# Kernel optimization log

Hardware: AMD Instinct MI355X
Metric: run time of the kernel (lower is better)

The kernel has to match this reference:

```python
import jax, jax.numpy as jnp
import numpy as np

B, L, D_MODEL = 2, 1024, 1024
D_STATE, D_CONV, EXPAND = 16, 4, 2
D_INNER = D_MODEL * EXPAND
LN_EPS = 1e-5


def setup_inputs() -> dict:
    key = jax.random.key(0)
    ks = jax.random.split(key, 6)
    g = lambda k, shape, scale: (jax.random.normal(k, shape, jnp.float32) * scale)
    x = jax.random.normal(ks[0], (B, L, D_MODEL), jnp.float32)
    in_proj_w = g(ks[1], (2 * D_INNER, D_MODEL), D_MODEL ** -0.5)
    conv_w = g(ks[2], (D_INNER, D_CONV), D_CONV ** -0.5)   # depthwise kernel
    conv_b = jnp.zeros((D_INNER,), jnp.float32)
    x_proj_w = g(ks[3], (2 * D_STATE + 1, D_INNER), D_INNER ** -0.5)
    A_log = jnp.tile(jnp.log(jnp.arange(1, D_STATE + 1, dtype=jnp.float32)), (D_INNER, 1))
    D_param = jnp.ones((D_INNER,), jnp.float32)
    dt_w = g(ks[4], (D_INNER, 1), 1.0)
    dt_b = jnp.full((D_INNER,), -4.0, jnp.float32)
    out_w = g(ks[5], (D_MODEL, D_INNER), D_INNER ** -0.5)
    ln_g = jnp.ones((D_INNER,), jnp.float32)
    ln_b = jnp.zeros((D_INNER,), jnp.float32)
    return dict(x=x, in_proj_w=in_proj_w, conv_w=conv_w, conv_b=conv_b,
                x_proj_w=x_proj_w, A_log=A_log, D_param=D_param,
                dt_w=dt_w, dt_b=dt_b, out_w=out_w, ln_g=ln_g, ln_b=ln_b)


def _forward(x, in_proj_w, conv_w, conv_b, x_proj_w, A_log, D_param,
             dt_w, dt_b, out_w, ln_g, ln_b):
    Lq = x.shape[1]
    xz = jnp.einsum('bld,ed->ble', x, in_proj_w)            # (B,L,2*Di)
    xb, z = xz[..., :D_INNER], xz[..., D_INNER:]
    # causal depthwise conv1d (pad left d_conv-1, valid conv == torch pad+truncate)
    xpad = jnp.pad(xb, ((0, 0), (D_CONV - 1, 0), (0, 0)))
    xc = conv_b
    for k in range(D_CONV):
        xc = xc + xpad[:, k:k + Lq, :] * conv_w[:, k]
    xb = jax.nn.silu(xc)
    proj = jnp.einsum('bld,ed->ble', xb, x_proj_w)          # (B,L,2N+1)
    dt_in = proj[..., :1]
    Bp = proj[..., 1:1 + D_STATE]                            # (B,L,N)
    Cp = proj[..., 1 + D_STATE:]                             # (B,L,N)
    dt = jax.nn.softplus(dt_in * dt_w[:, 0] + dt_b)          # (B,L,Di)
    A = -jnp.exp(A_log)                                      # (Di,N)
    dA = jnp.exp(dt[..., None] * A)                          # (B,L,Di,N)
    x_scaled = (xb * dt)[..., None] * Bp[..., None, :]       # (B,L,Di,N)
    # linear recurrence h[t] = dA[t]*h[t-1] + x_scaled[t] via associative scan
    def comb(a, b):
        return (a[0] * b[0], b[0] * a[1] + b[1])
    _, h = jax.lax.associative_scan(comb, (dA, x_scaled), axis=1)
    y = jnp.einsum('bldn,bln->bld', h, Cp) + xb * D_param    # (B,L,Di)
    mu = jnp.mean(y, axis=-1, keepdims=True)
    var = jnp.var(y, axis=-1, keepdims=True)
    y = (y - mu) / jnp.sqrt(var + LN_EPS) * ln_g + ln_b
    y = y * jax.nn.silu(z)
    return jnp.einsum('bld,ed->ble', y, out_w)               # (B,L,d_model)


def reference(x, in_proj_w, conv_w, conv_b, x_proj_w, A_log, D_param,
              dt_w, dt_b, out_w, ln_g, ln_b):
    return _forward(x, in_proj_w, conv_w, conv_b, x_proj_w, A_log, D_param,
                    dt_w, dt_b, out_w, ln_g, ln_b)
```

## Files before the change

### kernel.cpp

```cpp
#include <hip/hip_runtime.h>

typedef unsigned short u16;
typedef unsigned int u32;
typedef __bf16 bf16x8 __attribute__((ext_vector_type(8)));
typedef float f32x4 __attribute__((ext_vector_type(4)));
typedef unsigned short ushort8 __attribute__((ext_vector_type(8)));

__device__ __forceinline__ float bf2f(u16 b) {
    return __uint_as_float(((u32)b) << 16);
}
__device__ __forceinline__ u16 f2bf(float f) {
    u32 u = __float_as_uint(f);
    return (u16)((u + 0x7fffu + ((u >> 16) & 1u)) >> 16);
}

#define P_CONVW 0
#define P_CONVB 8192
#define P_ALOG  10240
#define P_DPAR  43008
#define P_DTW   45056
#define P_DTB   47104
#define P_LNG   49152
#define P_LNB   51200
#define P_TOTAL 53248

#define CCH 32
#define CT  32
#define CHUNKTOT 2097152
#define PSTRIDE 128

#define CV_X   524288
#define CV_W1  1572864
#define CV_TOT 2097152

struct ParamPtrs { const void* p[8]; };

__global__ __launch_bounds__(256) void canon_all(ParamPtrs pp, float* __restrict__ cpar,
                                                 const void* __restrict__ sx,
                                                 const void* __restrict__ sw1,
                                                 const void* __restrict__ swo,
                                                 u16* __restrict__ cx,
                                                 const void* __restrict__ sxp,
                                                 u16* __restrict__ wpad,
                                                 float* __restrict__ proj,
                                                 float* __restrict__ dout,
                                                 const u16* __restrict__ dp) {
    const bool isbf = (dp[0] != 0);
    const int blk = blockIdx.x;
    const int tid = threadIdx.x;
    if (blk < 8192) {
        const int i = blk * 256 + tid;
        const void* src;
        int off;
        if (i < CV_X)       { src = sx;  off = i; }
        else if (i < CV_W1) { src = sw1; off = i - CV_X; }
        else                { src = swo; off = i - CV_W1; }
        if (isbf) {
            ((uint2*)cx)[i] = ((const uint2*)src)[off];
        } else {
            const float4 v = ((const float4*)src)[off];
            uint2 o;
            o.x = (u32)f2bf(v.x) | ((u32)f2bf(v.y) << 16);
            o.y = (u32)f2bf(v.z) | ((u32)f2bf(v.w) << 16);
            ((uint2*)cx)[i] = o;
        }
    } else if (blk < 8400) {
        const int i = (blk - 8192) * 256 + tid;
        int seg, off;
        if (i < P_CONVB)      { seg = 0; off = i; }
        else if (i < P_ALOG)  { seg = 1; off = i - P_CONVB; }
        else if (i < P_DPAR)  { seg = 2; off = i - P_ALOG; }
        else if (i < P_DTW)   { seg = 3; off = i - P_DPAR; }
        else if (i < P_DTB)   { seg = 4; off = i - P_DTW; }
        else if (i < P_LNG)   { seg = 5; off = i - P_DTB; }
        else if (i < P_LNB)   { seg = 6; off = i - P_LNG; }
        else                  { seg = 7; off = i - P_LNB; }
        cpar[i] = isbf ? bf2f(((const u16*)pp.p[seg])[off]) : ((const float*)pp.p[seg])[off];
    } else if (blk < 8656) {
        const int i = (blk - 8400) * 256 + tid;
        const int idx = i * 4;
        const int row = idx >> 11;
        u16 o[4];
#pragma unroll
        for (int q = 0; q < 4; ++q) {
            float v = 0.f;
            if (row < 33)
                v = isbf ? bf2f(((const u16*)sxp)[idx + q]) : ((const float*)sxp)[idx + q];
            o[q] = f2bf(v);
        }
        *(uint2*)&wpad[idx] = *(uint2*)o;
    } else if (blk < 8912) {
        const int i = (blk - 8656) * 256 + tid;
        ((float4*)proj)[i] = make_float4(0.f, 0.f, 0.f, 0.f);
    } else {
        const int i = (blk - 8912) * 256 + tid;
        ((float4*)dout)[i] = make_float4(0.f, 0.f, 0.f, 0.f);
    }
}

template <int MODE>
__global__ __launch_bounds__(256) void gemm_bt(const u16* __restrict__ A,
                                               const u16* __restrict__ Bw,
                                               void* __restrict__ C,
                                               int M, int N, int Kseg,
                                               int lda, int ldb) {
    const int bm = blockIdx.x;
    const int bn = blockIdx.y;
    const int kbase = blockIdx.z * Kseg;
    const int tid = threadIdx.x;
    const int lane = tid & 63;
    const int wave = tid >> 6;
    const int wm = wave >> 1, wn = wave & 1;
    const int l16 = lane & 15, quad = lane >> 4;

    __shared__ __align__(16) u16 sA[128 * 32];
    __shared__ __align__(16) u16 sB[128 * 32];

    f32x4 acc[4][4] = {};

    const int rsub = lane >> 2;
    const int csub = (lane & 3) * 8;

    for (int k0 = 0; k0 < Kseg; k0 += 32) {
        const int kc = kbase + k0 + csub;
        __syncthreads();
#pragma unroll
        for (int q = 0; q < 2; ++q) {
            const int g = wave + 4 * q;
            const int row = g * 16 + rsub;
            __builtin_amdgcn_global_load_lds(
                (const u32*)&A[(size_t)(bm * 128 + row) * lda + kc],
                (u32*)&sA[g * 512], 16, 0, 0);
            __builtin_amdgcn_global_load_lds(
                (const u32*)&Bw[(size_t)(bn * 128 + row) * ldb + kc],
                (u32*)&sB[g * 512], 16, 0, 0);
        }
        __syncthreads();

        bf16x8 af[4], bg[4];
#pragma unroll
        for (int t = 0; t < 4; ++t) {
            af[t] = *(const bf16x8*)&sA[(wm * 64 + t * 16 + l16) * 32 + quad * 8];
            bg[t] = *(const bf16x8*)&sB[(wn * 64 + t * 16 + l16) * 32 + quad * 8];
        }
#pragma unroll
        for (int mt = 0; mt < 4; ++mt)
#pragma unroll
            for (int nt = 0; nt < 4; ++nt)
                acc[mt][nt] = __builtin_amdgcn_mfma_f32_16x16x32_bf16(
                    af[mt], bg[nt], acc[mt][nt], 0, 0, 0);
    }

    float* Cf = (float*)C + (MODE == 1 ? (size_t)blockIdx.z * M * N : (size_t)0);
#pragma unroll
    for (int mt = 0; mt < 4; ++mt) {
#pragma unroll
        for (int r = 0; r < 4; ++r) {
            const int row = bm * 128 + wm * 64 + mt * 16 + quad * 4 + r;
#pragma unroll
            for (int nt = 0; nt < 4; ++nt) {
                const int col = bn * 128 + wn * 64 + nt * 16 + l16;
                if (MODE == 0)
                    ((u16*)C)[(size_t)row * N + col] = f2bf(acc[mt][nt][r]);
                else if (MODE == 1)
                    Cf[(size_t)row * N + col] = acc[mt][nt][r];
                else
                    unsafeAtomicAdd(&Cf[(size_t)row * N + col], acc[mt][nt][r]);
            }
        }
    }
}

__global__ __launch_bounds__(256) void conv_silu(const u16* __restrict__ xz,
                                                 const float* __restrict__ par,
                                                 u16* __restrict__ xb16) {
    const int idx = blockIdx.x * 256 + threadIdx.x;
    const int d8 = idx & 255;
    const int bl = idx >> 8;
    const int l = bl & 1023;
    const int d0 = d8 * 8;

    float acc[8];
    {
        const float4 b0 = *(const float4*)&par[P_CONVB + d0];
        const float4 b1 = *(const float4*)&par[P_CONVB + d0 + 4];
        acc[0] = b0.x; acc[1] = b0.y; acc[2] = b0.z; acc[3] = b0.w;
        acc[4] = b1.x; acc[5] = b1.y; acc[6] = b1.z; acc[7] = b1.w;
    }
    float warr[8][4];
#pragma unroll
    for (int q = 0; q < 8; ++q) {
        const float4 w = *(const float4*)&par[P_CONVW + (d0 + q) * 4];
        warr[q][0] = w.x; warr[q][1] = w.y; warr[q][2] = w.z; warr[q][3] = w.w;
    }
#pragma unroll
    for (int k = 0; k < 4; ++k) {
        const int ls = l + k - 3;
        if (ls >= 0) {
            const ushort8 xv = *(const ushort8*)&xz[(size_t)(bl + k - 3) * 4096 + d0];
#pragma unroll
            for (int q = 0; q < 8; ++q)
                acc[q] = fmaf(bf2f(xv[q]), warr[q][k], acc[q]);
        }
    }
    u16 o[8];
#pragma unroll
    for (int q = 0; q < 8; ++q) {
        const float s = acc[q] / (1.f + __expf(-acc[q]));
        o[q] = f2bf(s);
    }
    *(uint4*)&xb16[(size_t)bl * 2048 + d0] = *(uint4*)o;
}

__global__ __launch_bounds__(256) void scan_p1(const u16* __restrict__ xb16,
                                               const float* __restrict__ proj,
                                               const float* __restrict__ par,
                                               float* __restrict__ PS) {
    const int d = blockIdx.x * 256 + threadIdx.x;
    const int c = blockIdx.y;
    const int b = blockIdx.z;
    __shared__ float sp[CT][33];
    const size_t row0 = (size_t)b * 1024 + c * CT;
    for (int f = threadIdx.x; f < CT * 33; f += 256) {
        const int i = f / 33, j = f - i * 33;
        sp[i][j] = proj[(row0 + i) * PSTRIDE + j];
    }
    float Aneg[16];
#pragma unroll
    for (int n = 0; n < 16; ++n) Aneg[n] = -__expf(par[P_ALOG + d * 16 + n]);
    const float dtw = par[P_DTW + d], dtb = par[P_DTB + d];
    __syncthreads();

    float h[16] = {}, P[16];
#pragma unroll
    for (int n = 0; n < 16; ++n) P[n] = 1.f;

    float xv = bf2f(xb16[row0 * 2048 + d]);
    for (int i = 0; i < CT; ++i) {
        const float xv_next = (i + 1 < CT) ? bf2f(xb16[(row0 + i + 1) * 2048 + d]) : 0.f;
        const float dtin = sp[i][0];
        const float darg = fmaf(dtin, dtw, dtb);
        const float dt = (darg > 20.f) ? darg : __logf(1.f + __expf(darg));
        const float xdt = xv * dt;
#pragma unroll
        for (int n = 0; n < 16; ++n) {
            const float dA = __expf(dt * Aneg[n]);
            P[n] *= dA;
            h[n] = fmaf(dA, h[n], xdt * sp[i][1 + n]);
        }
        xv = xv_next;
    }
    const size_t base = (((size_t)b * CCH + c) * 16) * 2048 + d;
#pragma unroll
    for (int n = 0; n < 16; ++n) {
        PS[base + (size_t)n * 2048] = P[n];
        PS[CHUNKTOT + base + (size_t)n * 2048] = h[n];
    }
}

__global__ __launch_bounds__(256) void scan_comb(const float* __restrict__ PS,
                                                 float* __restrict__ H) {
    const int t = blockIdx.x * 256 + threadIdx.x;
    const int d = t & 2047;
    const int n = (t >> 11) & 15;
    const int b = t >> 15;
    float h = 0.f;
#pragma unroll
    for (int c = 0; c < CCH; ++c) {
        const size_t idx = (((size_t)b * CCH + c) * 16 + n) * 2048 + d;
        H[idx] = h;
        h = fmaf(PS[idx], h, PS[CHUNKTOT + idx]);
    }
}

__global__ __launch_bounds__(256) void scan_p2(const u16* __restrict__ xb16,
                                               const float* __restrict__ proj,
                                               const float* __restrict__ par,
                                               const float* __restrict__ H,
                                               u16* __restrict__ y) {
    const int d = blockIdx.x * 256 + threadIdx.x;
    const int c = blockIdx.y;
    const int b = blockIdx.z;
    __shared__ float sp[CT][33];
    const size_t row0 = (size_t)b * 1024 + c * CT;
    for (int f = threadIdx.x; f < CT * 33; f += 256) {
        const int i = f / 33, j = f - i * 33;
        sp[i][j] = proj[(row0 + i) * PSTRIDE + j];
    }
    float Aneg[16], h[16];
    const size_t hbase = (((size_t)b * CCH + c) * 16) * 2048 + d;
#pragma unroll
    for (int n = 0; n < 16; ++n) {
        Aneg[n] = -__expf(par[P_ALOG + d * 16 + n]);
        h[n] = H[hbase + (size_t)n * 2048];
    }
    const float dtw = par[P_DTW + d], dtb = par[P_DTB + d];
    const float Dp = par[P_DPAR + d];
    __syncthreads();

    float xv = bf2f(xb16[row0 * 2048 + d]);
    for (int i = 0; i < CT; ++i) {
        const float xv_next = (i + 1 < CT) ? bf2f(xb16[(row0 + i + 1) * 2048 + d]) : 0.f;
        const float dtin = sp[i][0];
        const float darg = fmaf(dtin, dtw, dtb);
        const float dt = (darg > 20.f) ? darg : __logf(1.f + __expf(darg));
        const float xdt = xv * dt;
        float acc = 0.f;
#pragma unroll
        for (int n = 0; n < 16; ++n) {
            const float dA = __expf(dt * Aneg[n]);
            h[n] = fmaf(dA, h[n], xdt * sp[i][1 + n]);
            acc = fmaf(h[n], sp[i][17 + n], acc);
        }
        y[(row0 + i) * 2048 + d] = f2bf(fmaf(xv, Dp, acc));
        xv = xv_next;
    }
}

__global__ __launch_bounds__(256) void ln_silu(const u16* __restrict__ y,
                                               const u16* __restrict__ xz,
                                               const float* __restrict__ par,
                                               u16* __restrict__ yn) {
    const int row = blockIdx.x;
    const int tid = threadIdx.x;
    const int lane = tid & 63, wave = tid >> 6;
    const int d0 = tid * 8;
    const ushort8 vy = *(const ushort8*)&y[(size_t)row * 2048 + d0];
    float v[8];
    float s = 0.f, s2 = 0.f;
#pragma unroll
    for (int i = 0; i < 8; ++i) {
        v[i] = bf2f(vy[i]);
        s += v[i];
        s2 = fmaf(v[i], v[i], s2);
    }
    s += __shfl_xor(s, 1); s2 += __shfl_xor(s2, 1);
    s += __shfl_xor(s, 2); s2 += __shfl_xor(s2, 2);
    s += __shfl_xor(s, 4); s2 += __shfl_xor(s2, 4);
    s += __shfl_xor(s, 8); s2 += __shfl_xor(s2, 8);
    s += __shfl_xor(s, 16); s2 += __shfl_xor(s2, 16);
    s += __shfl_xor(s, 32); s2 += __shfl_xor(s2, 32);
    __shared__ float rs[4], rs2[4];
    if (lane == 0) { rs[wave] = s; rs2[wave] = s2; }
    __syncthreads();
    const float ts = rs[0] + rs[1] + rs[2] + rs[3];
    const float ts2 = rs2[0] + rs2[1] + rs2[2] + rs2[3];
    const float mu = ts * (1.f / 2048.f);
    const float var = ts2 * (1.f / 2048.f) - mu * mu;
    const float rstd = rsqrtf(var + 1e-5f);

    const ushort8 vz = *(const ushort8*)&xz[(size_t)row * 4096 + 2048 + d0];
    float g[8], bb[8];
    {
        const float4 g0 = *(const float4*)&par[P_LNG + d0];
        const float4 g1 = *(const float4*)&par[P_LNG + d0 + 4];
        g[0] = g0.x; g[1] = g0.y; g[2] = g0.z; g[3] = g0.w;
        g[4] = g1.x; g[5] = g1.y; g[6] = g1.z; g[7] = g1.w;
        const float4 b0 = *(const float4*)&par[P_LNB + d0];
        const float4 b1 = *(const float4*)&par[P_LNB + d0 + 4];
        bb[0] = b0.x; bb[1] = b0.y; bb[2] = b0.z; bb[3] = b0.w;
        bb[4] = b1.x; bb[5] = b1.y; bb[6] = b1.z; bb[7] = b1.w;
    }
    u16 o[8];
#pragma unroll
    for (int i = 0; i < 8; ++i) {
        float t = (v[i] - mu) * rstd * g[i] + bb[i];
        const float z = bf2f(vz[i]);
        t *= z / (1.f + __expf(-z));
        o[i] = f2bf(t);
    }
    *(uint4*)&yn[(size_t)row * 2048 + d0] = *(uint4*)o;
}

extern "C" void kernel_launch(void* const* d_in, const int* in_sizes, int n_in,
                              void* d_out, int out_size, void* d_ws, size_t ws_size,
                              hipStream_t stream) {
    const void* x         = d_in[0];
    const void* in_proj_w = d_in[1];
    const void* conv_w    = d_in[2];
    const void* conv_b    = d_in[3];
    const void* x_proj_w  = d_in[4];
    const void* A_log     = d_in[5];
    const void* D_param   = d_in[6];
    const void* dt_w      = d_in[7];
    const void* dt_b      = d_in[8];
    const void* out_w     = d_in[9];
    const void* ln_g      = d_in[10];
    const void* ln_b      = d_in[11];
    const u16* dp = (const u16*)D_param;

    float* cpar = (float*)d_ws;
    u16* cx     = (u16*)(cpar + P_TOTAL);
    u16* cw1    = cx + 2097152;
    u16* cwo    = cw1 + 4194304;
    u16* xz     = cwo + 2097152;
    u16* xb16   = xz + 8388608;
    u16* y      = xb16 + 4194304;
    u16* wpad   = y + 4194304;
    float* proj = (float*)(wpad + 262144);
    float* PS   = proj + 262144;
    float* H    = PS + 2 * CHUNKTOT;
    u16* yn     = xb16;

    ParamPtrs pp;
    pp.p[0] = conv_w; pp.p[1] = conv_b; pp.p[2] = A_log; pp.p[3] = D_param;
    pp.p[4] = dt_w;   pp.p[5] = dt_b;   pp.p[6] = ln_g;  pp.p[7] = ln_b;
    canon_all<<<10960, 256, 0, stream>>>(pp, cpar, x, in_proj_w, out_w, cx,
                                         x_proj_w, wpad, proj, (float*)d_out, dp);

    gemm_bt<0><<<dim3(16, 32, 1), 256, 0, stream>>>(cx, cw1, xz, 2048, 4096, 1024, 1024, 1024);
    conv_silu<<<2048, 256, 0, stream>>>(xz, cpar, xb16);
    gemm_bt<2><<<dim3(16, 1, 8), 256, 0, stream>>>(xb16, wpad, proj, 2048, 128, 256, 2048, 2048);
    scan_p1<<<dim3(8, CCH, 2), 256, 0, stream>>>(xb16, proj, cpar, PS);
    scan_comb<<<256, 256, 0, stream>>>(PS, H);
    scan_p2<<<dim3(8, CCH, 2), 256, 0, stream>>>(xb16, proj, cpar, H, y);
    ln_silu<<<2048, 256, 0, stream>>>(y, xz, cpar, yn);
    gemm_bt<2><<<dim3(16, 8, 2), 256, 0, stream>>>(yn, cwo, (float*)d_out, 2048, 1024, 1024, 2048, 2048);
}
```

Before: 255.4 us.

## Add triple-buffered direct-to-LDS GEMM and replace atomic split-K with partial reductions

Adds a new 512-thread GEMM kernel that loads tiles straight into swizzled LDS through global_load_lds, keeps three LDS stages in flight, and interleaves fragment reads with MFMA under raised wave priority. It uses 128x256 tiles and is used for the input and output projections. Split-K results for x_proj and out_proj are now written as separate partial buffers and summed by a new reduce kernel, replacing float atomics and the zero-init in canon_all. The cost is more LDS per block (144KB), extra workspace for the partials, and two extra kernel launches.

```diff
diff --git a/kernel.cpp b/kernel.cpp
--- a/kernel.cpp
+++ b/kernel.cpp
@@ -42,8 +42,6 @@
                                                  u16* __restrict__ cx,
                                                  const void* __restrict__ sxp,
                                                  u16* __restrict__ wpad,
-                                                 float* __restrict__ proj,
-                                                 float* __restrict__ dout,
                                                  const u16* __restrict__ dp) {
     const bool isbf = (dp[0] != 0);
     const int blk = blockIdx.x;
@@ -76,7 +74,7 @@
         else if (i < P_LNB)   { seg = 6; off = i - P_LNG; }
         else                  { seg = 7; off = i - P_LNB; }
         cpar[i] = isbf ? bf2f(((const u16*)pp.p[seg])[off]) : ((const float*)pp.p[seg])[off];
-    } else if (blk < 8656) {
+    } else {
         const int i = (blk - 8400) * 256 + tid;
         const int idx = i * 4;
         const int row = idx >> 11;
@@ -89,12 +87,132 @@
             o[q] = f2bf(v);
         }
         *(uint2*)&wpad[idx] = *(uint2*)o;
-    } else if (blk < 8912) {
-        const int i = (blk - 8656) * 256 + tid;
-        ((float4*)proj)[i] = make_float4(0.f, 0.f, 0.f, 0.f);
-    } else {
-        const int i = (blk - 8912) * 256 + tid;
-        ((float4*)dout)[i] = make_float4(0.f, 0.f, 0.f, 0.f);
+    }
+}
+
+__device__ __forceinline__ bf16x8 lds_frag(const char* smem, u32 base, int row, int kk,
+                                           int quad, u32 xorv) {
+    const u32 addr = (base + (u32)(row * 128 + kk * 64 + quad * 16)) ^ xorv;
+    return *(const bf16x8*)(smem + addr);
+}
+
+template <int MODE>
+__global__ __launch_bounds__(512, 2) void gemm8(const u16* __restrict__ A,
+                                                const u16* __restrict__ Bw,
+                                                void* __restrict__ C,
+                                                int M, int N, int Kseg,
+                                                int lda, int ldb) {
+    extern __shared__ char smem[];
+    const int bm = blockIdx.x, bn = blockIdx.y;
+    const int kbase = blockIdx.z * Kseg;
+    const int tid = threadIdx.x;
+    const int lane = tid & 63, wave = tid >> 6;
+    const int wm = wave >> 2, wn = wave & 3;
+    const int l16 = lane & 15, quad = lane >> 4;
+    const int NT = Kseg >> 6;
+    const u32 xorv = (u32)((l16 & 7) << 4);
+
+    const int rIss = wave * 8 + (lane >> 3);
+    const int logC = (lane & 7) ^ ((lane >> 3) & 7);
+    size_t aSrc[2], bSrc[4];
+#pragma unroll
+    for (int j = 0; j < 2; ++j)
+        aSrc[j] = (size_t)(bm * 128 + j * 64 + rIss) * lda + logC * 8 + kbase;
+#pragma unroll
+    for (int j = 0; j < 4; ++j)
+        bSrc[j] = (size_t)(bn * 256 + j * 64 + rIss) * ldb + logC * 8 + kbase;
+    const u32 ldsW = (u32)(wave * 1024);
+
+#define SG_A(slot, j, kel) __builtin_amdgcn_global_load_lds( \
+        (const u32*)(A + aSrc[j] + (kel)), (u32*)(smem + (slot) + (j) * 8192 + ldsW), 16, 0, 0)
+#define SG_B(slot, j, kel) __builtin_amdgcn_global_load_lds( \
+        (const u32*)(Bw + bSrc[j] + (kel)), (u32*)(smem + (slot) + (j) * 8192 + ldsW), 16, 0, 0)
+
+    const u32 sA0 = 0, sA1 = 16384, sA2 = 32768;
+    const u32 sB0 = 49152, sB1 = 81920, sB2 = 114688;
+
+    SG_A(sA0, 0, 0); SG_A(sA0, 1, 0);
+    SG_B(sB0, 0, 0); SG_B(sB0, 1, 0); SG_B(sB0, 2, 0); SG_B(sB0, 3, 0);
+    SG_A(sA1, 0, 64); SG_A(sA1, 1, 64);
+    SG_B(sB1, 0, 64); SG_B(sB1, 1, 64); SG_B(sB1, 2, 64); SG_B(sB1, 3, 64);
+    asm volatile("s_waitcnt vmcnt(6)" ::: "memory");
+    __builtin_amdgcn_s_barrier();
+    __builtin_amdgcn_sched_barrier(0);
+
+    u32 curA = sA0, nxtA = sA1, stgA = sA2;
+    u32 curB = sB0, nxtB = sB1, stgB = sB2;
+    int kStage = 128;
+
+    f32x4 acc[4][4] = {};
+    bf16x8 a[4][2], b[4][2];
+
+    for (int t = 0; t < NT; ++t) {
+        const bool doStage = (t + 2) < NT;
+#pragma unroll
+        for (int mt = 0; mt < 4; ++mt)
+#pragma unroll
+            for (int kk = 0; kk < 2; ++kk)
+                a[mt][kk] = lds_frag(smem, curA, wm * 64 + mt * 16 + l16, kk, quad, xorv);
+#pragma unroll
+        for (int nt = 0; nt < 2; ++nt)
+#pragma unroll
+            for (int kk = 0; kk < 2; ++kk)
+                b[nt][kk] = lds_frag(smem, curB, wn * 64 + nt * 16 + l16, kk, quad, xorv);
+        if (doStage) { SG_A(stgA, 0, kStage); SG_A(stgA, 1, kStage); SG_B(stgB, 0, kStage); }
+        __builtin_amdgcn_s_setprio(1);
+#pragma unroll
+        for (int mt = 0; mt < 4; ++mt)
+#pragma unroll
+            for (int nt = 0; nt < 2; ++nt)
+#pragma unroll
+                for (int kk = 0; kk < 2; ++kk)
+                    acc[mt][nt] = __builtin_amdgcn_mfma_f32_16x16x32_bf16(
+                        a[mt][kk], b[nt][kk], acc[mt][nt], 0, 0, 0);
+        __builtin_amdgcn_s_setprio(0);
+#pragma unroll
+        for (int nt = 2; nt < 4; ++nt)
+#pragma unroll
+            for (int kk = 0; kk < 2; ++kk)
+                b[nt][kk] = lds_frag(smem, curB, wn * 64 + nt * 16 + l16, kk, quad, xorv);
+        if (doStage) { SG_B(stgB, 1, kStage); SG_B(stgB, 2, kStage); SG_B(stgB, 3, kStage); }
+        __builtin_amdgcn_s_setprio(1);
+#pragma unroll
+        for (int mt = 0; mt < 4; ++mt)
+#pragma unroll
+            for (int nt = 2; nt < 4; ++nt)
+#pragma unroll
+                for (int kk = 0; kk < 2; ++kk)
+                    acc[mt][nt] = __builtin_amdgcn_mfma_f32_16x16x32_bf16(
+                        a[mt][kk], b[nt][kk], acc[mt][nt], 0, 0, 0);
+        __builtin_amdgcn_s_setprio(0);
+        if (t < NT - 1) {
+            if (doStage) asm volatile("s_waitcnt vmcnt(6)" ::: "memory");
+            else         asm volatile("s_waitcnt vmcnt(0)" ::: "memory");
+            __builtin_amdgcn_s_barrier();
+            __builtin_amdgcn_sched_barrier(0);
+            u32 tA = curA; curA = nxtA; nxtA = stgA; stgA = tA;
+            u32 tB = curB; curB = nxtB; nxtB = stgB; stgB = tB;
+            kStage += 64;
+        }
+    }
+#undef SG_A
+#undef SG_B
+
+    float* Cf = (float*)C + (MODE == 1 ? (size_t)blockIdx.z * M * N : (size_t)0);
+#pragma unroll
+    for (int mt = 0; mt < 4; ++mt) {
+#pragma unroll
+        for (int r = 0; r < 4; ++r) {
+            const int row = bm * 128 + wm * 64 + mt * 16 + quad * 4 + r;
+#pragma unroll
+            for (int nt = 0; nt < 4; ++nt) {
+                const int col = bn * 256 + wn * 64 + nt * 16 + l16;
+                if (MODE == 0)
+                    ((u16*)C)[(size_t)row * N + col] = f2bf(acc[mt][nt][r]);
+                else
+                    Cf[(size_t)row * N + col] = acc[mt][nt][r];
+            }
+        }
     }
 }
 
@@ -162,13 +280,24 @@
                 const int col = bn * 128 + wn * 64 + nt * 16 + l16;
                 if (MODE == 0)
                     ((u16*)C)[(size_t)row * N + col] = f2bf(acc[mt][nt][r]);
-                else if (MODE == 1)
+                else
                     Cf[(size_t)row * N + col] = acc[mt][nt][r];
-                else
-                    unsafeAtomicAdd(&Cf[(size_t)row * N + col], acc[mt][nt][r]);
             }
         }
     }
+}
+
+__global__ __launch_bounds__(256) void reduce_parts(const float* __restrict__ src,
+                                                    float* __restrict__ dst,
+                                                    int n4, int parts) {
+    const int i = blockIdx.x * 256 + threadIdx.x;
+    if (i >= n4) return;
+    float4 s = ((const float4*)src)[i];
+    for (int p = 1; p < parts; ++p) {
+        const float4 v = ((const float4*)src)[(size_t)p * n4 + i];
+        s.x += v.x; s.y += v.y; s.z += v.z; s.w += v.w;
+    }
+    ((float4*)dst)[i] = s;
 }
 
 __global__ __launch_bounds__(256) void conv_silu(const u16* __restrict__ xz,
@@ -400,20 +529,35 @@
     float* proj = (float*)(wpad + 262144);
     float* PS   = proj + 262144;
     float* H    = PS + 2 * CHUNKTOT;
-    u16* yn     = xb16;
+    float* gpart = H + CHUNKTOT;
+    float* xpart = (float*)cx;
+    u16* yn      = xb16;
+
+    static bool attrSet = false;
+    if (!attrSet) {
+        hipFuncSetAttribute(reinterpret_cast<const void*>(&gemm8<0>),
+                            hipFuncAttributeMaxDynamicSharedMemorySize, 147456);
+        hipFuncSetAttribute(reinterpret_cast<const void*>(&gemm8<1>),
+                            hipFuncAttributeMaxDynamicSharedMemorySize, 147456);
+        attrSet = true;
+    }
 
     ParamPtrs pp;
     pp.p[0] = conv_w; pp.p[1] = conv_b; pp.p[2] = A_log; pp.p[3] = D_param;
     pp.p[4] = dt_w;   pp.p[5] = dt_b;   pp.p[6] = ln_g;  pp.p[7] = ln_b;
-    canon_all<<<10960, 256, 0, stream>>>(pp, cpar, x, in_proj_w, out_w, cx,
-                                         x_proj_w, wpad, proj, (float*)d_out, dp);
-
-    gemm_bt<0><<<dim3(16, 32, 1), 256, 0, stream>>>(cx, cw1, xz, 2048, 4096, 1024, 1024, 1024);
+    canon_all<<<8656, 256, 0, stream>>>(pp, cpar, x, in_proj_w, out_w, cx,
+                                        x_proj_w, wpad, dp);
+
+    gemm8<0><<<dim3(16, 16, 1), 512, 147456, stream>>>(cx, cw1, xz,
+                                                       2048, 4096, 1024, 1024, 1024);
     conv_silu<<<2048, 256, 0, stream>>>(xz, cpar, xb16);
-    gemm_bt<2><<<dim3(16, 1, 8), 256, 0, stream>>>(xb16, wpad, proj, 2048, 128, 256, 2048, 2048);
+    gemm_bt<1><<<dim3(16, 1, 8), 256, 0, stream>>>(xb16, wpad, xpart, 2048, 128, 256, 2048, 2048);
+    reduce_parts<<<256, 256, 0, stream>>>(xpart, proj, 65536, 8);
     scan_p1<<<dim3(8, CCH, 2), 256, 0, stream>>>(xb16, proj, cpar, PS);
     scan_comb<<<256, 256, 0, stream>>>(PS, H);
     scan_p2<<<dim3(8, CCH, 2), 256, 0, stream>>>(xb16, proj, cpar, H, y);
     ln_silu<<<2048, 256, 0, stream>>>(y, xz, cpar, yn);
-    gemm_bt<2><<<dim3(16, 8, 2), 256, 0, stream>>>(yn, cwo, (float*)d_out, 2048, 1024, 1024, 2048, 2048);
-}
+    gemm8<1><<<dim3(16, 4, 4), 512, 147456, stream>>>(yn, cwo, gpart,
+                                                      2048, 1024, 512, 2048, 2048);
+    reduce_parts<<<2048, 256, 0, stream>>>(gpart, (float*)d_out, 524288, 4);
+}
```

New measurement: 241.5 us. 5.5% less time.
